# Kernel optimization log

Measured on AMD Instinct MI355X. Metric: run time of the kernel, lower is better.

The kernel has to match this reference:

```python
import jax, jax.numpy as jnp
import numpy as np
from jax import lax


def _conv(x, w, padding):
    # NCHW input, OIHW weights, stride 1, no bias
    return lax.conv_general_dilated(x, w, (1, 1), padding,
                                    dimension_numbers=('NCHW', 'OIHW', 'NCHW'))


def setup_inputs() -> dict:
    key = jax.random.key(0)
    ks = jax.random.split(key, 6)
    B, C, H, W = 16, 512, 40, 40
    return {
        'exemplar': jax.random.normal(ks[0], (B, C, H, W), jnp.float32),
        'query':    jax.random.normal(ks[1], (B, C, H, W), jnp.float32),
        'w_e':  jax.random.normal(ks[2], (256, C, 1, 1), jnp.float32) * 0.01,
        'w_q':  jax.random.normal(ks[3], (256, C, 1, 1), jnp.float32) * 0.01,
        'w_c1': jax.random.normal(ks[4], (C, C, 3, 3), jnp.float32) * 0.01,
        'w_c2': jax.random.normal(ks[5], (C, C, 3, 3), jnp.float32) * 0.01,
    }


def reference(exemplar, query, w_e, w_q, w_c1, w_c2):
    B, C, H, W = query.shape
    N = H * W
    # 1x1 projections to 256-dim correlation space
    q_corr = _conv(query, w_q, 'VALID').reshape(B, -1, N)     # [B,256,N]
    e_corr = _conv(exemplar, w_e, 'VALID').reshape(B, -1, N)  # [B,256,N]
    # A[b, n_exemplar, m_query] = <e_corr[:, n], q_corr[:, m]>
    A = jnp.einsum('bcn,bcm->bnm', e_corr, q_corr)            # [B,N,N]
    # A1 = softmax over exemplar axis, then transpose (torch: softmax(A,dim=1).T)
    A1 = jnp.swapaxes(jax.nn.softmax(A, axis=1), 1, 2)        # [B,N,N]
    # Bm = softmax(A^T, dim=1).T  == softmax(A, axis=2)
    Bm = jnp.swapaxes(jax.nn.softmax(jnp.swapaxes(A, 1, 2), axis=1), 1, 2)
    e_flat = exemplar.reshape(B, C, N)
    q_flat = query.reshape(B, C, N)
    query_att = jnp.matmul(e_flat, A1)   # [B,C,N]
    exemplar_att = jnp.matmul(q_flat, Bm)  # [B,C,N]
    input1_att = _conv(exemplar_att.reshape(B, C, H, W), w_c1, 'SAME')
    input2_att = _conv(query_att.reshape(B, C, H, W), w_c2, 'SAME')
    return jnp.concatenate([input1_att, input2_att], axis=1)  # [B,2C,H,W]
```

## Files before the change

kernel.cpp:

```cpp
#include <hip/hip_runtime.h>

typedef unsigned short u16;
typedef __attribute__((ext_vector_type(8))) short bf16x8;
typedef __attribute__((ext_vector_type(4))) float f32x4;

__device__ __forceinline__ u16 f2bf(float f) {
  union { float f; unsigned u; } v; v.f = f;
  unsigned u = v.u;
  u += 0x7fffu + ((u >> 16) & 1u);
  return (u16)(u >> 16);
}

__device__ __forceinline__ void gll16(const void* g, void* l) {
  __builtin_amdgcn_global_load_lds(
      (const __attribute__((address_space(1))) void*)g,
      (__attribute__((address_space(3))) void*)l, 16, 0, 0);
}

__global__ __launch_bounds__(256) void transp_cast_x2(const float* __restrict__ ex,
                                                      const float* __restrict__ qu,
                                                      u16* __restrict__ xte,
                                                      u16* __restrict__ xtq) {
  __shared__ float t[32][33];
  int z = blockIdx.z;
  int b = z & 15;
  const float* xb = (z < 16 ? ex : qu) + (size_t)b * 819200;
  u16* xtb = (z < 16 ? xte : xtq) + (size_t)b * 819200;
  int n0 = blockIdx.x * 32, c0 = blockIdx.y * 32;
  int tx = threadIdx.x & 31, ty = threadIdx.x >> 5;
#pragma unroll
  for (int k = 0; k < 4; k++) {
    int c = ty + k * 8;
    t[c][tx] = xb[(size_t)(c0 + c) * 1600 + n0 + tx];
  }
  __syncthreads();
#pragma unroll
  for (int k = 0; k < 4; k++) {
    int n = ty + k * 8;
    xtb[(size_t)(n0 + n) * 512 + c0 + tx] = f2bf(t[tx][n]);
  }
}

__global__ void cast_w(const float* __restrict__ we, const float* __restrict__ wq,
                       u16* __restrict__ oe, u16* __restrict__ oq) {
  int i = blockIdx.x * 256 + threadIdx.x;
  oe[i] = f2bf(we[i]);
  oq[i] = f2bf(wq[i]);
}

__global__ void repack_wc(const float* __restrict__ w1, const float* __restrict__ w2,
                          u16* __restrict__ o1, u16* __restrict__ o2) {
  const float* w = blockIdx.y ? w2 : w1;
  u16* wr = blockIdx.y ? o2 : o1;
  int idx = blockIdx.x * 256 + threadIdx.x;
  int o = idx / 4608;
  int r = idx - o * 4608;
  int t = r >> 9;
  int c = r & 511;
  wr[idx] = f2bf(w[o * 4608 + c * 9 + t]);
}

__global__ void zero_mem(uint4* __restrict__ p, long n) {
  long i = (long)blockIdx.x * blockDim.x + threadIdx.x;
  long stride = (long)gridDim.x * blockDim.x;
  uint4 z; z.x = 0; z.y = 0; z.z = 0; z.w = 0;
  for (; i < n; i += stride) p[i] = z;
}

template <int MODE>
__global__ __launch_bounds__(256) void gemm_bt64(
    const u16* __restrict__ A, const u16* __restrict__ B, u16* __restrict__ C,
    const u16* __restrict__ A2, const u16* __restrict__ B2, u16* __restrict__ C2,
    int M, int N, int K, long sA, long sB, long sC) {
  __shared__ u16 lds_a[128 * 64];
  __shared__ u16 lds_b[128 * 64];
  int tid = threadIdx.x;
  int z = blockIdx.z, b = z & 15;
  const u16* Ab = (z < 16 ? A : A2) + (size_t)b * sA;
  const u16* Bb = (z < 16 ? B : B2) + (size_t)b * sB;
  u16* Cb = (z < 16 ? C : C2) + (size_t)b * sC;
  int m0 = blockIdx.x * 128, n0 = blockIdx.y * 128;

  int rsub = tid >> 3;
  int gch = (tid & 7) ^ (rsub & 7);
  long Kb = (long)K * 2;
  const char* pa[4];
  const char* pb[4];
#pragma unroll
  for (int c = 0; c < 4; c++) {
    int ra = m0 + 32 * c + rsub; ra = ra < M ? ra : M - 1;
    int rb = n0 + 32 * c + rsub; rb = rb < N ? rb : N - 1;
    pa[c] = (const char*)Ab + (long)ra * Kb + gch * 16;
    pb[c] = (const char*)Bb + (long)rb * Kb + gch * 16;
  }

  const f32x4 fzero = {0.f, 0.f, 0.f, 0.f};
  f32x4 acc[4][4];
#pragma unroll
  for (int mi = 0; mi < 4; mi++)
#pragma unroll
    for (int ni = 0; ni < 4; ni++) acc[mi][ni] = fzero;

  int wid = tid >> 6, lane = tid & 63;
  int wm = wid & 1, wn = wid >> 1;
  int lrow = lane & 15, lquad = lane >> 4;
  int sl = lrow & 7;

  int ksteps = K >> 6;
  for (int ks = 0; ks < ksteps; ks++) {
#pragma unroll
    for (int c = 0; c < 4; c++) {
      gll16(pa[c], (char*)lds_a + c * 4096 + tid * 16);
      gll16(pb[c], (char*)lds_b + c * 4096 + tid * 16);
      pa[c] += 128; pb[c] += 128;
    }
    __syncthreads();
#pragma unroll
    for (int k2 = 0; k2 < 2; k2++) {
      int sel = ((k2 << 2) | lquad) ^ sl;
      bf16x8 bv[4];
#pragma unroll
      for (int ni = 0; ni < 4; ni++) {
        int rowb = wn * 64 + ni * 16 + lrow;
        bv[ni] = *(const bf16x8*)((const char*)lds_b + rowb * 128 + sel * 16);
      }
#pragma unroll
      for (int mi = 0; mi < 4; mi++) {
        int rowa = wm * 64 + mi * 16 + lrow;
        bf16x8 av = *(const bf16x8*)((const char*)lds_a + rowa * 128 + sel * 16);
#pragma unroll
        for (int ni = 0; ni < 4; ni++)
          acc[mi][ni] =
              __builtin_amdgcn_mfma_f32_16x16x32_bf16(av, bv[ni], acc[mi][ni], 0, 0, 0);
      }
    }
    __syncthreads();
  }

#pragma unroll
  for (int mi = 0; mi < 4; mi++) {
#pragma unroll
    for (int r = 0; r < 4; r++) {
      int i = m0 + wm * 64 + mi * 16 + lquad * 4 + r;
      if (i >= M) continue;
#pragma unroll
      for (int ni = 0; ni < 4; ni++) {
        int j = n0 + wn * 64 + ni * 16 + lrow;
        if (j >= N) continue;
        float v = acc[mi][ni][r];
        if (MODE == 2) {
          int y = i / 40, x = i - y * 40;
          Cb[(size_t)((y + 1) * 42 + (x + 1)) * 512 + j] = f2bf(v);
        } else {
          Cb[(size_t)i * N + j] = f2bf(v);
        }
      }
    }
  }
}

__global__ __launch_bounds__(256) void gemm_corr_exp(
    const u16* __restrict__ A, const u16* __restrict__ B, u16* __restrict__ E,
    u16* __restrict__ ET, float* __restrict__ Zrow, float* __restrict__ Zcol) {
  __shared__ u16 lds_a[128 * 64];
  __shared__ u16 lds_b[128 * 64];
  int tid = threadIdx.x;
  int b = blockIdx.z;
  const u16* Ab = A + (size_t)b * 409600;
  const u16* Bb = B + (size_t)b * 409600;
  u16* Eb = E + (size_t)b * 2560000;
  u16* ETb = ET + (size_t)b * 2560000;
  int m0 = blockIdx.x * 128, n0 = blockIdx.y * 128;

  int rsub = tid >> 3;
  int gch = (tid & 7) ^ (rsub & 7);
  const char* pa[4];
  const char* pb[4];
#pragma unroll
  for (int c = 0; c < 4; c++) {
    int ra = m0 + 32 * c + rsub; ra = ra < 1600 ? ra : 1599;
    int rb = n0 + 32 * c + rsub; rb = rb < 1600 ? rb : 1599;
    pa[c] = (const char*)(Ab + (size_t)ra * 256) + gch * 16;
    pb[c] = (const char*)(Bb + (size_t)rb * 256) + gch * 16;
  }

  const f32x4 fzero = {0.f, 0.f, 0.f, 0.f};
  f32x4 acc[4][4];
#pragma unroll
  for (int mi = 0; mi < 4; mi++)
#pragma unroll
    for (int ni = 0; ni < 4; ni++) acc[mi][ni] = fzero;

  int wid = tid >> 6, lane = tid & 63;
  int wm = wid & 1, wn = wid >> 1;
  int lrow = lane & 15, lquad = lane >> 4;
  int sl = lrow & 7;

  for (int ks = 0; ks < 4; ks++) {
#pragma unroll
    for (int c = 0; c < 4; c++) {
      gll16(pa[c], (char*)lds_a + c * 4096 + tid * 16);
      gll16(pb[c], (char*)lds_b + c * 4096 + tid * 16);
      pa[c] += 128; pb[c] += 128;
    }
    __syncthreads();
#pragma unroll
    for (int k2 = 0; k2 < 2; k2++) {
      int sel = ((k2 << 2) | lquad) ^ sl;
      bf16x8 bv[4];
#pragma unroll
      for (int ni = 0; ni < 4; ni++) {
        int rowb = wn * 64 + ni * 16 + lrow;
        bv[ni] = *(const bf16x8*)((const char*)lds_b + rowb * 128 + sel * 16);
      }
#pragma unroll
      for (int mi = 0; mi < 4; mi++) {
        int rowa = wm * 64 + mi * 16 + lrow;
        bf16x8 av = *(const bf16x8*)((const char*)lds_a + rowa * 128 + sel * 16);
#pragma unroll
        for (int ni = 0; ni < 4; ni++)
          acc[mi][ni] =
              __builtin_amdgcn_mfma_f32_16x16x32_bf16(av, bv[ni], acc[mi][ni], 0, 0, 0);
      }
    }
    __syncthreads();
  }

  const int TS = 136;
  u16* T = lds_a;
  float colacc[4] = {0.f, 0.f, 0.f, 0.f};
#pragma unroll
  for (int s = 0; s < 4; s++) {
    if (wm == (s >> 1)) {
      int smi0 = (s & 1) * 2;
#pragma unroll
      for (int mi2 = 0; mi2 < 2; mi2++) {
        int mi = smi0 + mi2;
        float rowp[4] = {0.f, 0.f, 0.f, 0.f};
#pragma unroll
        for (int ni = 0; ni < 4; ni++) {
          int j = n0 + wn * 64 + ni * 16 + lrow;
          bool jv = j < 1600;
#pragma unroll
          for (int r = 0; r < 4; r++) {
            int i = m0 + wm * 64 + mi * 16 + lquad * 4 + r;
            float e = __expf(acc[mi][ni][r]);
            T[(mi2 * 16 + lquad * 4 + r) * TS + wn * 64 + ni * 16 + lrow] = f2bf(e);
            rowp[r] += jv ? e : 0.f;
            colacc[ni] += (i < 1600) ? e : 0.f;
          }
        }
#pragma unroll
        for (int r = 0; r < 4; r++) {
          float v = rowp[r];
          v += __shfl_xor(v, 1);
          v += __shfl_xor(v, 2);
          v += __shfl_xor(v, 4);
          v += __shfl_xor(v, 8);
          int i = m0 + wm * 64 + mi * 16 + lquad * 4 + r;
          if (lrow == 0 && i < 1600) atomicAdd(&Zrow[b * 1600 + i], v);
        }
      }
    }
    __syncthreads();
#pragma unroll
    for (int p = 0; p < 2; p++) {
      int jj = tid + p * 256;
      int ml = jj >> 4, n8 = jj & 15;
      int gi = m0 + s * 32 + ml, gj = n0 + n8 * 8;
      if (gi < 1600 && gj < 1600)
        *(uint4*)(Eb + (size_t)gi * 1600 + gj) = *(const uint4*)&T[ml * TS + n8 * 8];
    }
#pragma unroll
    for (int p = 0; p < 4; p++) {
      int jj = tid + p * 256;
      int n = jj >> 3, m4 = jj & 7;
      int gm = m0 + s * 32 + m4 * 4, gn = n0 + n;
      if (gn < 1600 && gm < 1600) {
        ushort4 v;
        v.x = T[(m4 * 4 + 0) * TS + n];
        v.y = T[(m4 * 4 + 1) * TS + n];
        v.z = T[(m4 * 4 + 2) * TS + n];
        v.w = T[(m4 * 4 + 3) * TS + n];
        *(ushort4*)(ETb + (size_t)gn * 1600 + gm) = v;
      }
    }
    __syncthreads();
  }
#pragma unroll
  for (int ni = 0; ni < 4; ni++) {
    float v = colacc[ni];
    v += __shfl_xor(v, 16);
    v += __shfl_xor(v, 32);
    int j = n0 + wn * 64 + ni * 16 + lrow;
    if (lquad == 0 && j < 1600) atomicAdd(&Zcol[b * 1600 + j], v);
  }
}

__global__ void scale_div(const float* __restrict__ ex, const float* __restrict__ qu,
                          const float* __restrict__ Zcol, const float* __restrict__ Zrow,
                          u16* __restrict__ ebf, u16* __restrict__ qbf) {
  const float* x; const float* Z; u16* o;
  if (blockIdx.y == 0) { x = ex; Z = Zcol; o = ebf; }
  else { x = qu; Z = Zrow; o = qbf; }
  size_t idx = (size_t)blockIdx.x * 256 + threadIdx.x;
  int b = (int)(idx / 819200);
  int i = (int)(idx % 1600);
  o[idx] = f2bf(x[idx] / Z[b * 1600 + i]);
}

__global__ __launch_bounds__(256) void conv_gemm64(
    const u16* __restrict__ W1, const u16* __restrict__ ATT1,
    const u16* __restrict__ W2, const u16* __restrict__ ATT2,
    float* __restrict__ out) {
  __shared__ u16 lds_a[128 * 64];
  __shared__ u16 lds_b[128 * 64];
  int tid = threadIdx.x;
  int z = blockIdx.z, b = z & 15, sel2 = z >> 4;
  const u16* W = sel2 ? W2 : W1;
  const u16* attb = (sel2 ? ATT2 : ATT1) + (size_t)b * 903168;
  float* outb = out + (size_t)b * 1638400 + (size_t)(sel2 ? 512 : 0) * 1600;
  int p0 = blockIdx.x * 128, o0 = blockIdx.y * 128;

  int rsub = tid >> 3;
  int gch = (tid & 7) ^ (rsub & 7);
  const char* pa[4];
  const char* pb[4];
#pragma unroll
  for (int c = 0; c < 4; c++) {
    int ro = o0 + 32 * c + rsub;
    pa[c] = (const char*)(W + (size_t)ro * 4608) + gch * 16;
    int p = p0 + 32 * c + rsub; p = p < 1600 ? p : 1599;
    int y = p / 40, x = p - y * 40;
    pb[c] = (const char*)(attb + (size_t)(y * 42 + x) * 512) + gch * 16;
  }

  const f32x4 fzero = {0.f, 0.f, 0.f, 0.f};
  f32x4 acc[4][4];
#pragma unroll
  for (int mi = 0; mi < 4; mi++)
#pragma unroll
    for (int ni = 0; ni < 4; ni++) acc[mi][ni] = fzero;

  int wid = tid >> 6, lane = tid & 63;
  int wm = wid & 1, wn = wid >> 1;
  int lrow = lane & 15, lquad = lane >> 4;
  int sl = lrow & 7;

  int tapbyte = 0, dxc = 0;
  for (int t = 0; t < 9; t++) {
#pragma unroll 2
    for (int kc = 0; kc < 8; kc++) {
#pragma unroll
      for (int c = 0; c < 4; c++) {
        gll16(pa[c], (char*)lds_a + c * 4096 + tid * 16);
        gll16(pb[c] + tapbyte + kc * 128, (char*)lds_b + c * 4096 + tid * 16);
        pa[c] += 128;
      }
      __syncthreads();
#pragma unroll
      for (int k2 = 0; k2 < 2; k2++) {
        int sel = ((k2 << 2) | lquad) ^ sl;
        bf16x8 bv[4];
#pragma unroll
        for (int ni = 0; ni < 4; ni++) {
          int rowb = wn * 64 + ni * 16 + lrow;
          bv[ni] = *(const bf16x8*)((const char*)lds_b + rowb * 128 + sel * 16);
        }
#pragma unroll
        for (int mi = 0; mi < 4; mi++) {
          int rowa = wm * 64 + mi * 16 + lrow;
          bf16x8 av = *(const bf16x8*)((const char*)lds_a + rowa * 128 + sel * 16);
#pragma unroll
          for (int ni = 0; ni < 4; ni++)
            acc[mi][ni] = __builtin_amdgcn_mfma_f32_16x16x32_bf16(av, bv[ni],
                                                                  acc[mi][ni], 0, 0, 0);
        }
      }
      __syncthreads();
    }
    dxc++;
    tapbyte += 1024;
    if (dxc == 3) { dxc = 0; tapbyte += 39 * 1024; }
  }

#pragma unroll
  for (int mi = 0; mi < 4; mi++) {
#pragma unroll
    for (int r = 0; r < 4; r++) {
      int o = o0 + wm * 64 + mi * 16 + lquad * 4 + r;
#pragma unroll
      for (int ni = 0; ni < 4; ni++) {
        int p = p0 + wn * 64 + ni * 16 + lrow;
        if (p < 1600) outb[(size_t)o * 1600 + p] = acc[mi][ni][r];
      }
    }
  }
}

extern "C" void kernel_launch(void* const* d_in, const int* in_sizes, int n_in,
                              void* d_out, int out_size, void* d_ws, size_t ws_size,
                              hipStream_t stream) {
  const float* ex = (const float*)d_in[0];
  const float* qu = (const float*)d_in[1];
  const float* w_e = (const float*)d_in[2];
  const float* w_q = (const float*)d_in[3];
  const float* w_c1 = (const float*)d_in[4];
  const float* w_c2 = (const float*)d_in[5];
  float* out = (float*)d_out;
  char* ws = (char*)d_ws;

  u16* E     = (u16*)(ws + 0L);
  u16* ET    = (u16*)(ws + 81920000L);
  u16* xt_e  = (u16*)(ws + 163840000L);
  u16* xt_q  = (u16*)(ws + 190054400L);
  u16* ecorr = (u16*)(ws + 216268800L);
  u16* qcorr = (u16*)(ws + 229376000L);
  u16* att_e = (u16*)(ws + 242483200L);
  u16* att_q = (u16*)(ws + 271384576L);
  float* Zrow = (float*)(ws + 300285952L);
  float* Zcol = (float*)(ws + 300388352L);
  u16* w_ebf = (u16*)(ws + 300490752L);
  u16* w_qbf = (u16*)(ws + 300752896L);
  u16* wr1   = (u16*)(ws + 301015040L);
  u16* wr2   = (u16*)(ws + 305733632L);

  transp_cast_x2<<<dim3(50, 16, 32), 256, 0, stream>>>(ex, qu, xt_e, xt_q);
  cast_w<<<dim3(512), 256, 0, stream>>>(w_e, w_q, w_ebf, w_qbf);
  repack_wc<<<dim3(9216, 2), 256, 0, stream>>>(w_c1, w_c2, wr1, wr2);
  zero_mem<<<dim3(2048), 256, 0, stream>>>((uint4*)att_e, 3625472L);

  gemm_bt64<0><<<dim3(13, 2, 32), 256, 0, stream>>>(
      xt_e, w_ebf, ecorr, xt_q, w_qbf, qcorr, 1600, 256, 512, 819200L, 0L, 409600L);

  gemm_corr_exp<<<dim3(13, 13, 16), 256, 0, stream>>>(ecorr, qcorr, E, ET, Zrow, Zcol);

  u16* ebf = xt_e;
  u16* qbf = xt_q;
  scale_div<<<dim3(51200, 2), 256, 0, stream>>>(ex, qu, Zcol, Zrow, ebf, qbf);

  gemm_bt64<2><<<dim3(13, 4, 32), 256, 0, stream>>>(
      E, ebf, att_q, ET, qbf, att_e, 1600, 512, 1600, 2560000L, 819200L, 903168L);

  conv_gemm64<<<dim3(13, 4, 32), 256, 0, stream>>>(wr1, att_e, wr2, att_q, out);
}
```

Measured before the change: 918.8 us.

## Vectorize auxiliary kernels, zero only borders and Z buffers, add launch bounds

```diff
diff --git a/kernel.cpp b/kernel.cpp
--- a/kernel.cpp
+++ b/kernel.cpp
@@ -21,23 +21,30 @@
                                                       const float* __restrict__ qu,
                                                       u16* __restrict__ xte,
                                                       u16* __restrict__ xtq) {
-  __shared__ float t[32][33];
+  __shared__ float t[64][65];
   int z = blockIdx.z;
   int b = z & 15;
   const float* xb = (z < 16 ? ex : qu) + (size_t)b * 819200;
   u16* xtb = (z < 16 ? xte : xtq) + (size_t)b * 819200;
-  int n0 = blockIdx.x * 32, c0 = blockIdx.y * 32;
-  int tx = threadIdx.x & 31, ty = threadIdx.x >> 5;
-#pragma unroll
-  for (int k = 0; k < 4; k++) {
-    int c = ty + k * 8;
-    t[c][tx] = xb[(size_t)(c0 + c) * 1600 + n0 + tx];
+  int n0 = blockIdx.x * 64, c0 = blockIdx.y * 64;
+  int n = threadIdx.x & 63, cq = threadIdx.x >> 6;
+#pragma unroll
+  for (int r = 0; r < 16; r++) {
+    int c = cq + r * 4;
+    t[c][n] = xb[(size_t)(c0 + c) * 1600 + n0 + n];
   }
   __syncthreads();
-#pragma unroll
-  for (int k = 0; k < 4; k++) {
-    int n = ty + k * 8;
-    xtb[(size_t)(n0 + n) * 512 + c0 + tx] = f2bf(t[tx][n]);
+  int cg = threadIdx.x & 15, nr = threadIdx.x >> 4;
+#pragma unroll
+  for (int r = 0; r < 4; r++) {
+    int nn = nr + r * 16;
+    int c = cg * 4;
+    ushort4 v;
+    v.x = f2bf(t[c + 0][nn]);
+    v.y = f2bf(t[c + 1][nn]);
+    v.z = f2bf(t[c + 2][nn]);
+    v.w = f2bf(t[c + 3][nn]);
+    *(ushort4*)&xtb[(size_t)(n0 + nn) * 512 + c0 + c] = v;
   }
 }
 
@@ -48,27 +55,39 @@
   oq[i] = f2bf(wq[i]);
 }
 
-__global__ void repack_wc(const float* __restrict__ w1, const float* __restrict__ w2,
-                          u16* __restrict__ o1, u16* __restrict__ o2) {
+__global__ void repack_wc2(const float* __restrict__ w1, const float* __restrict__ w2,
+                           u16* __restrict__ o1, u16* __restrict__ o2) {
   const float* w = blockIdx.y ? w2 : w1;
   u16* wr = blockIdx.y ? o2 : o1;
   int idx = blockIdx.x * 256 + threadIdx.x;
-  int o = idx / 4608;
-  int r = idx - o * 4608;
-  int t = r >> 9;
-  int c = r & 511;
-  wr[idx] = f2bf(w[o * 4608 + c * 9 + t]);
-}
-
-__global__ void zero_mem(uint4* __restrict__ p, long n) {
-  long i = (long)blockIdx.x * blockDim.x + threadIdx.x;
-  long stride = (long)gridDim.x * blockDim.x;
+  int o = idx >> 9, c = idx & 511;
+  const float* src = w + (size_t)idx * 9;
+  float v[9];
+#pragma unroll
+  for (int t = 0; t < 9; t++) v[t] = src[t];
+#pragma unroll
+  for (int t = 0; t < 9; t++) wr[o * 4608 + t * 512 + c] = f2bf(v[t]);
+}
+
+__global__ void zero_small(uint4* __restrict__ p) {
   uint4 z; z.x = 0; z.y = 0; z.z = 0; z.w = 0;
-  for (; i < n; i += stride) p[i] = z;
+  p[blockIdx.x * 256 + threadIdx.x] = z;
+}
+
+__global__ void zero_border(u16* __restrict__ att_e, u16* __restrict__ att_q) {
+  u16* base = (blockIdx.z ? att_q : att_e) + (size_t)blockIdx.y * 903168;
+  int k = blockIdx.x * 4 + (threadIdx.x >> 6);
+  int y, x;
+  if (k < 42) { y = 0; x = k; }
+  else if (k < 84) { y = 41; x = k - 42; }
+  else { int r = k - 84; y = 1 + (r >> 1); x = (r & 1) ? 41 : 0; }
+  int lane = threadIdx.x & 63;
+  uint4 z; z.x = 0; z.y = 0; z.z = 0; z.w = 0;
+  *(uint4*)(base + (size_t)(y * 42 + x) * 512 + lane * 8) = z;
 }
 
 template <int MODE>
-__global__ __launch_bounds__(256) void gemm_bt64(
+__global__ __launch_bounds__(256, 4) void gemm_bt64(
     const u16* __restrict__ A, const u16* __restrict__ B, u16* __restrict__ C,
     const u16* __restrict__ A2, const u16* __restrict__ B2, u16* __restrict__ C2,
     int M, int N, int K, long sA, long sB, long sC) {
@@ -297,19 +316,26 @@
   }
 }
 
-__global__ void scale_div(const float* __restrict__ ex, const float* __restrict__ qu,
-                          const float* __restrict__ Zcol, const float* __restrict__ Zrow,
-                          u16* __restrict__ ebf, u16* __restrict__ qbf) {
+__global__ void scale_div4(const float* __restrict__ ex, const float* __restrict__ qu,
+                           const float* __restrict__ Zcol, const float* __restrict__ Zrow,
+                           u16* __restrict__ ebf, u16* __restrict__ qbf) {
   const float* x; const float* Z; u16* o;
   if (blockIdx.y == 0) { x = ex; Z = Zcol; o = ebf; }
   else { x = qu; Z = Zrow; o = qbf; }
-  size_t idx = (size_t)blockIdx.x * 256 + threadIdx.x;
-  int b = (int)(idx / 819200);
-  int i = (int)(idx % 1600);
-  o[idx] = f2bf(x[idx] / Z[b * 1600 + i]);
-}
-
-__global__ __launch_bounds__(256) void conv_gemm64(
+  size_t e = ((size_t)blockIdx.x * 256 + threadIdx.x) * 4;
+  int b = (int)(e / 819200);
+  int i = (int)(e % 1600);
+  float4 x4 = *(const float4*)(x + e);
+  float4 z4 = *(const float4*)(Z + b * 1600 + i);
+  ushort4 v;
+  v.x = f2bf(x4.x / z4.x);
+  v.y = f2bf(x4.y / z4.y);
+  v.z = f2bf(x4.z / z4.z);
+  v.w = f2bf(x4.w / z4.w);
+  *(ushort4*)(o + e) = v;
+}
+
+__global__ __launch_bounds__(256, 4) void conv_gemm64(
     const u16* __restrict__ W1, const u16* __restrict__ ATT1,
     const u16* __restrict__ W2, const u16* __restrict__ ATT2,
     float* __restrict__ out) {
@@ -425,10 +451,11 @@
   u16* wr1   = (u16*)(ws + 301015040L);
   u16* wr2   = (u16*)(ws + 305733632L);
 
-  transp_cast_x2<<<dim3(50, 16, 32), 256, 0, stream>>>(ex, qu, xt_e, xt_q);
+  transp_cast_x2<<<dim3(25, 8, 32), 256, 0, stream>>>(ex, qu, xt_e, xt_q);
   cast_w<<<dim3(512), 256, 0, stream>>>(w_e, w_q, w_ebf, w_qbf);
-  repack_wc<<<dim3(9216, 2), 256, 0, stream>>>(w_c1, w_c2, wr1, wr2);
-  zero_mem<<<dim3(2048), 256, 0, stream>>>((uint4*)att_e, 3625472L);
+  repack_wc2<<<dim3(1024, 2), 256, 0, stream>>>(w_c1, w_c2, wr1, wr2);
+  zero_small<<<dim3(50), 256, 0, stream>>>((uint4*)Zrow);
+  zero_border<<<dim3(41, 16, 2), 256, 0, stream>>>(att_e, att_q);
 
   gemm_bt64<0><<<dim3(13, 2, 32), 256, 0, stream>>>(
       xt_e, w_ebf, ecorr, xt_q, w_qbf, qcorr, 1600, 256, 512, 819200L, 0L, 409600L);
@@ -437,7 +464,7 @@
 
   u16* ebf = xt_e;
   u16* qbf = xt_q;
-  scale_div<<<dim3(51200, 2), 256, 0, stream>>>(ex, qu, Zcol, Zrow, ebf, qbf);
+  scale_div4<<<dim3(12800, 2), 256, 0, stream>>>(ex, qu, Zcol, Zrow, ebf, qbf);
 
   gemm_bt64<2><<<dim3(13, 4, 32), 256, 0, stream>>>(
       E, ebf, att_q, ET, qbf, att_e, 1600, 512, 1600, 2560000L, 819200L, 903168L);
```

Result: slower. 1.164 ms (+26.6%).
